# Performance work log

Hardware: AMD Instinct MI355X
Metric: run time of the kernel (lower is better)

The kernel has to match this reference:

```python
import jax, jax.numpy as jnp
import numpy as np
import math

B, A, T = 64, 23, 128          # batch, num_agents, max seq len
D, AE, S, H = 256, 32, 6, 8    # d_model, agent_encoding_dim, static_dim, heads
DK = D // H                     # 32
DM = D + AE                     # 288, MHA q/k/v dim
NEG = -1e10                     # masked_fill constant from source


def sinusoidal_pe(pos, d):
    # pos: int array [...], returns [..., d] standard transformer PE at positions pos
    half = jnp.arange(d // 2, dtype=jnp.float32)
    div = jnp.exp(-half * (math.log(10000.0) * 2.0 / d))          # [d/2]
    ang = pos[..., None].astype(jnp.float32) * div                # [..., d/2]
    return jnp.stack([jnp.sin(ang), jnp.cos(ang)], axis=-1).reshape(*pos.shape, d)


def setup_inputs() -> dict:
    key = jax.random.key(0)
    ks = jax.random.split(key, 20)
    std = 0.02
    data = jax.random.normal(ks[0], (B, A, T), jnp.float32)
    lengths = jax.random.randint(ks[1], (B, A), 0, T + 1).astype(jnp.int32)   # mask arg = lengths
    t = jnp.arange(T, dtype=jnp.int32)
    time = jnp.where(t[None, None, :] < lengths[:, :, None], t[None, None, :], -1)  # [B,A,T], -1 = pad
    static = jax.random.normal(ks[2], (B, S), jnp.float32)
    # per-agent Linear(1, D): weight [A, D], bias [A, D]
    W_embed = std * jax.random.normal(ks[3], (A, D), jnp.float32)
    b_embed = std * jax.random.normal(ks[4], (A, D), jnp.float32)
    E_var = std * jax.random.normal(ks[5], (A, AE), jnp.float32)            # VariateEncoding table
    W_static = std * jax.random.normal(ks[6], (S, D), jnp.float32)
    b_static = jnp.zeros((D,), jnp.float32)
    Wq = std * jax.random.normal(ks[7], (DM, D), jnp.float32); bq = jnp.zeros((D,), jnp.float32)
    Wk = std * jax.random.normal(ks[8], (DM, D), jnp.float32); bk = jnp.zeros((D,), jnp.float32)
    Wv = std * jax.random.normal(ks[9], (DM, D), jnp.float32); bv = jnp.zeros((D,), jnp.float32)
    Wo = std * jax.random.normal(ks[10], (D, DM), jnp.float32); bo = jnp.zeros((DM,), jnp.float32)
    Wg = std * jax.random.normal(ks[11], (DM + D, 1), jnp.float32); bg = jnp.zeros((1,), jnp.float32)
    return dict(data=data, time=time, mask=lengths, static=static,
                W_embed=W_embed, b_embed=b_embed, E_var=E_var,
                W_static=W_static, b_static=b_static,
                Wq=Wq, bq=bq, Wk=Wk, bk=bk, Wv=Wv, bv=bv, Wo=Wo, bo=bo,
                Wg=Wg, bg=bg)


def reference(data, time, mask, static, W_embed, b_embed, E_var, W_static, b_static,
              Wq, bq, Wk, bk, Wv, bv, Wo, bo, Wg, bg):
    lengths = mask                                            # [B,A] sequence lengths
    t = jnp.arange(T)
    valid = t[None, None, :] < lengths[:, :, None]            # [B,A,T] bool
    # mask_matrix[i,:len,:len]=1 double loop -> vectorized outer product
    mask4 = valid[:, :, :, None] & valid[:, :, None, :]       # [B,A,T,T]

    # per-agent Linear(1, D) loop -> batched rank-1 affine, then ReLU
    data_embeds = jax.nn.relu(data[..., None] * W_embed[None, :, None, :]
                              + b_embed[None, :, None, :])    # [B,A,T,D]

    # src_pe: sinusoidal positional encoding at (clamped) time values
    pe = sinusoidal_pe(jnp.maximum(time, 0), D)               # [B,A,T,D]
    src = data_embeds + pe

    # variate (agent-id) embedding concat -> [B,A,T,D+AE]; encoder = identity
    var = jnp.broadcast_to(E_var[None, :, None, :], (B, A, T, AE))
    memory = jnp.concatenate([src, var], axis=-1)             # [B,A,T,DM]

    # time-masked mean pool over T
    time_mask = time >= 0                                     # [B,A,T]
    memory = jnp.where(time_mask[..., None], memory, 0.0)
    counts = time_mask.sum(axis=2).astype(memory.dtype)       # [B,A]
    agentwise = memory.sum(axis=2) / (counts[..., None] + 1e-9)  # [B,A,DM]

    # custom MHA (dim='Time'): q_len = 1 per agent, keys/values over T
    q = jnp.einsum('bae,ed->bad', agentwise, Wq) + bq          # [B,A,D]
    k = jnp.einsum('bate,ed->batd', memory, Wk) + bk           # [B,A,T,D]
    v = jnp.einsum('bate,ed->batd', memory, Wv) + bv
    qh = q.reshape(B, A, H, DK)                                # [B,A,H,DK] (q_len=1 squeezed)
    kh = k.reshape(B, A, T, H, DK).transpose(0, 1, 3, 2, 4)    # [B,A,H,T,DK]
    vh = v.reshape(B, A, T, H, DK).transpose(0, 1, 3, 2, 4)
    scores = jnp.einsum('bahd,bahtd->baht', qh, kh) / math.sqrt(DK)  # [B,A,H,T]
    amask = mask4[:, :, 0, :]                                  # [B,A,T] row 0 of per-agent mask
    scores = jnp.where(amask[:, :, None, :], scores, NEG)
    p = jax.nn.softmax(scores, axis=-1)                        # dropout = eval (identity)
    ctx = jnp.einsum('baht,bahtd->bahd', p, vh).reshape(B, A, D)
    agent_feat = jnp.einsum('bad,de->bae', ctx, Wo) + bo       # [B,A,DM]

    # agent-masked mean pool over agents
    agent_mask = counts > 0                                    # [B,A]
    agent_feat = jnp.where(agent_mask[..., None], agent_feat, 0.0)
    denom = agent_mask.sum(axis=1).astype(agent_feat.dtype) + 1e-9
    aggre = agent_feat.sum(axis=1) / denom[:, None]            # [B,DM]

    static_feat = static @ W_static + b_static                 # [B,D]
    all_feature = jnp.concatenate([aggre, static_feat], axis=-1)  # [B,DM+D]
    return all_feature @ Wg + bg                               # [B,1]


if __name__ == '__main__':
    out = reference(**setup_inputs())
    print(out.shape, jnp.asarray(out).dtype)
```

## Files before the change

### kernel.cpp

```cpp
#include <hip/hip_runtime.h>
#include <math.h>

#define NB 64
#define NA 23
#define NT 128
#define ND 256
#define NAE 32
#define NS 6
#define NH 8
#define NDM 288

#define OFF_PET    0
#define OFF_PECUM  32768
#define OFF_WKT    65792
#define OFF_VWO    131328
#define OFF_CST    133632
#define OFF_S      133648

__global__ __launch_bounds__(256) void setup_kernel(
    const float* __restrict__ Wk, const float* __restrict__ Wv,
    const float* __restrict__ Wo, const float* __restrict__ Wg,
    const float* __restrict__ bv, const float* __restrict__ bo,
    const float* __restrict__ W_static, const float* __restrict__ b_static,
    const float* __restrict__ bg, float* __restrict__ ws)
{
    const int blk = blockIdx.x;
    const int tid = threadIdx.x;
    float* peT   = ws + OFF_PET;
    float* PEcum = ws + OFF_PECUM;
    float* WkT   = ws + OFF_WKT;
    float* VWo   = ws + OFF_VWO;
    float* cst   = ws + OFF_CST;

    if (blk < 128) {
        const int g = tid >> 7, t = tid & 127;
        const int e = blk * 2 + g;
        const int i = e >> 1;
        const float kdiv = 0.07195578415606394f;
        const float dv = expf(-(float)i * kdiv);
        const float ang = (float)t * dv;
        const float v = (e & 1) ? cosf(ang) : sinf(ang);
        peT[e * NT + t] = v;
        __shared__ float buf[256];
        buf[tid] = v;
        #pragma unroll
        for (int s = 1; s < 128; s <<= 1) {
            __syncthreads();
            float add = (t >= s) ? buf[tid - s] : 0.f;
            __syncthreads();
            buf[tid] += add;
        }
        __syncthreads();
        PEcum[(t + 1) * ND + e] = buf[tid];
    } else if (blk < 384) {
        const int j = blk - 128;
        const float scale = 0.17677669529663687f;
        WkT[j * 256 + tid] = Wk[tid * ND + j] * scale;
    } else if (blk < 392) {
        const int h = blk - 384;
        __shared__ float wog[32];
        {
            const int jj = tid >> 3, sub = tid & 7;
            const int j = h * 32 + jj;
            float acc = 0.f;
            const int m0 = sub * 36;
            #pragma unroll 4
            for (int m = m0; m < m0 + 36; ++m)
                acc = fmaf(Wo[j * NDM + m], Wg[m], acc);
            acc += __shfl_down(acc, 4, 8);
            acc += __shfl_down(acc, 2, 8);
            acc += __shfl_down(acc, 1, 8);
            if (sub == 0) wog[jj] = acc;
        }
        __syncthreads();
        for (int e = tid; e < NDM; e += 256) {
            float acc = 0.f;
            #pragma unroll 8
            for (int jj = 0; jj < 32; ++jj)
                acc = fmaf(Wv[e * ND + h * 32 + jj], wog[jj], acc);
            VWo[h * NDM + e] = acc;
        }
        if (tid == 0) {
            float acc = 0.f;
            #pragma unroll 8
            for (int jj = 0; jj < 32; ++jj)
                acc = fmaf(bv[h * 32 + jj], wog[jj], acc);
            cst[8 + h] = acc;
        }
    } else {
        const int i = tid >> 5, sub = tid & 31;
        float acc = 0.f;
        if (i < 6) {
            for (int m = sub; m < 256; m += 32)
                acc = fmaf(W_static[i * ND + m], Wg[NDM + m], acc);
        } else if (i == 6) {
            for (int m = sub; m < 256; m += 32)
                acc = fmaf(b_static[m], Wg[NDM + m], acc);
        } else {
            for (int m = sub; m < NDM; m += 32)
                acc = fmaf(bo[m], Wg[m], acc);
        }
        #pragma unroll
        for (int off = 16; off > 0; off >>= 1)
            acc += __shfl_down(acc, off, 32);
        if (sub == 0) cst[i] = (i == 6) ? acc + bg[0] : acc;
    }
}

__global__ __launch_bounds__(256) void main_kernel(
    const float* __restrict__ data, const int* __restrict__ lengths,
    const float* __restrict__ W_embed, const float* __restrict__ b_embed,
    const float* __restrict__ E_var,
    const float* __restrict__ Wq, const float* __restrict__ bq,
    float* __restrict__ ws)
{
    const int wg = blockIdx.x;
    const int a = wg % NA;
    const int tid = threadIdx.x;
    const int L = lengths[wg];

    if (L == 0) {
        if (tid == 0) ws[OFF_S + wg] = 0.f;
        return;
    }

    __shared__ float xs[NT];
    __shared__ float agentwise[NDM];
    __shared__ float qs[ND];
    __shared__ float2 Wb[ND];
    __shared__ __align__(16) float combo[ND * 16];
    __shared__ float evvS[NH];
    __shared__ float red[4];

    const float* peT   = ws + OFF_PET;
    const float* PEcum = ws + OFF_PECUM;
    const float* WkT   = ws + OFF_WKT;
    const float* VWo   = ws + OFF_VWO;
    const float* cstp  = ws + OFF_CST;

    if (tid < NT) xs[tid] = data[wg * NT + tid];
    __syncthreads();
    {
        const int e = tid;
        const float We = W_embed[a * ND + e];
        const float be = b_embed[a * ND + e];
        Wb[e] = make_float2(We, be);
        float acc = 0.f;
        #pragma unroll 4
        for (int t = 0; t < L; ++t)
            acc += fmaxf(fmaf(xs[t], We, be), 0.f);
        agentwise[e] = (acc + PEcum[L * ND + e]) / (float)L;
    }
    if (tid < NAE) agentwise[ND + tid] = E_var[a * NAE + tid];
    __syncthreads();

    {
        const int j = tid;
        float acc = bq[j];
        #pragma unroll 4
        for (int f = 0; f < NDM; ++f)
            acc = fmaf(agentwise[f], Wq[f * ND + j], acc);
        qs[j] = acc;
    }
    __syncthreads();

    {
        const int h = tid >> 5, eo = tid & 31;
        const float* wr = WkT + (h * 32) * 256;
        for (int eb = 0; eb < 8; ++eb) {
            const int e = eb * 32 + eo;
            float acc = 0.f;
            #pragma unroll 8
            for (int j = 0; j < 32; ++j)
                acc = fmaf(wr[j * 256 + e], qs[h * 32 + j], acc);
            combo[e * 16 + h] = acc;
        }
    }
    for (int idx = tid; idx < NH * ND; idx += 256) {
        const int h = idx >> 8, e = idx & 255;
        combo[e * 16 + 8 + h] = VWo[h * NDM + e];
    }
    {
        const int h = tid >> 5, ee = tid & 31;
        float v = E_var[a * NAE + ee] * VWo[h * NDM + ND + ee];
        v += __shfl_down(v, 16, 32);
        v += __shfl_down(v, 8, 32);
        v += __shfl_down(v, 4, 32);
        v += __shfl_down(v, 2, 32);
        v += __shfl_down(v, 1, 32);
        if (ee == 0) evvS[h] = v;
    }
    __syncthreads();

    {
        const int t = tid & 127;
        const int half = tid >> 7;
        const float xt = xs[t];
        float accS[8], accM[8];
        #pragma unroll
        for (int h = 0; h < 8; ++h) { accS[h] = 0.f; accM[h] = 0.f; }
        const int ebase = half * 128;
        const float4* comboV = (const float4*)combo + ebase * 4;
        const float* peCol = peT + ebase * NT + t;
        #pragma unroll 2
        for (int ee = 0; ee < 128; ++ee) {
            const float2 wb = Wb[ebase + ee];
            const float m = fmaxf(fmaf(xt, wb.x, wb.y), 0.f) + peCol[ee * NT];
            const float4 c0 = comboV[ee * 4 + 0];
            const float4 c1 = comboV[ee * 4 + 1];
            const float4 c2 = comboV[ee * 4 + 2];
            const float4 c3 = comboV[ee * 4 + 3];
            accS[0] = fmaf(m, c0.x, accS[0]);
            accS[1] = fmaf(m, c0.y, accS[1]);
            accS[2] = fmaf(m, c0.z, accS[2]);
            accS[3] = fmaf(m, c0.w, accS[3]);
            accS[4] = fmaf(m, c1.x, accS[4]);
            accS[5] = fmaf(m, c1.y, accS[5]);
            accS[6] = fmaf(m, c1.z, accS[6]);
            accS[7] = fmaf(m, c1.w, accS[7]);
            accM[0] = fmaf(m, c2.x, accM[0]);
            accM[1] = fmaf(m, c2.y, accM[1]);
            accM[2] = fmaf(m, c2.z, accM[2]);
            accM[3] = fmaf(m, c2.w, accM[3]);
            accM[4] = fmaf(m, c3.x, accM[4]);
            accM[5] = fmaf(m, c3.y, accM[5]);
            accM[6] = fmaf(m, c3.z, accM[6]);
            accM[7] = fmaf(m, c3.w, accM[7]);
        }
        __syncthreads();
        float* sc   = combo;
        float* mvb  = combo + 1024;
        float* scP1 = combo + 2048;
        float* mvP1 = combo + 3072;
        if (half == 1) {
            #pragma unroll
            for (int h = 0; h < 8; ++h) {
                scP1[h * NT + t] = accS[h];
                mvP1[h * NT + t] = accM[h];
            }
        }
        __syncthreads();
        if (half == 0) {
            #pragma unroll
            for (int h = 0; h < 8; ++h) {
                sc[h * NT + t]  = accS[h] + scP1[h * NT + t];
                mvb[h * NT + t] = accM[h] + mvP1[h * NT + t];
            }
        }
    }
    __syncthreads();

    {
        const float* sc  = combo;
        const float* mvb = combo + 1024;
        const int wv = tid >> 6, lane = tid & 63;
        float wsum = 0.f;
        for (int hh = 0; hh < 2; ++hh) {
            const int h = wv * 2 + hh;
            float s1 = (lane < L) ? sc[h * NT + lane] : -3e38f;
            float s2 = (lane + 64 < L) ? sc[h * NT + 64 + lane] : -3e38f;
            float mx = fmaxf(s1, s2);
            #pragma unroll
            for (int off = 32; off > 0; off >>= 1)
                mx = fmaxf(mx, __shfl_down(mx, off, 64));
            mx = __shfl(mx, 0, 64);
            const float vbv = evvS[h] + cstp[8 + h];
            float e1 = (lane < L) ? __expf(s1 - mx) : 0.f;
            float e2 = (lane + 64 < L) ? __expf(s2 - mx) : 0.f;
            float num = e1 * (mvb[h * NT + lane] + vbv);
            num = fmaf(e2, mvb[h * NT + 64 + lane] + vbv, num);
            float den = e1 + e2;
            #pragma unroll
            for (int off = 32; off > 0; off >>= 1) {
                num += __shfl_down(num, off, 64);
                den += __shfl_down(den, off, 64);
            }
            if (lane == 0) wsum += num / den;
        }
        if (lane == 0) red[wv] = wsum;
    }
    __syncthreads();
    if (tid == 0) {
        ws[OFF_S + wg] = cstp[7] + red[0] + red[1] + red[2] + red[3];
    }
}

__global__ __launch_bounds__(64) void final_kernel(
    const float* __restrict__ statics, const int* __restrict__ lengths,
    const float* __restrict__ ws, float* __restrict__ out)
{
    const int b = threadIdx.x;
    const float* s_arr = ws + OFF_S;
    const float* cst = ws + OFF_CST;
    float sum = 0.f;
    int n = 0;
    for (int a = 0; a < NA; ++a) {
        if (lengths[b * NA + a] > 0) { sum += s_arr[b * NA + a]; ++n; }
    }
    float o = sum / ((float)n + 1e-9f);
    #pragma unroll
    for (int i = 0; i < NS; ++i)
        o = fmaf(statics[b * NS + i], cst[i], o);
    o += cst[6];
    out[b] = o;
}

extern "C" void kernel_launch(void* const* d_in, const int* in_sizes, int n_in,
                              void* d_out, int out_size, void* d_ws, size_t ws_size,
                              hipStream_t stream) {
    const float* data     = (const float*)d_in[0];
    const int*   mask     = (const int*)d_in[2];
    const float* statics  = (const float*)d_in[3];
    const float* W_embed  = (const float*)d_in[4];
    const float* b_embed  = (const float*)d_in[5];
    const float* E_var    = (const float*)d_in[6];
    const float* W_static = (const float*)d_in[7];
    const float* b_static = (const float*)d_in[8];
    const float* Wq       = (const float*)d_in[9];
    const float* bq       = (const float*)d_in[10];
    const float* Wk       = (const float*)d_in[11];
    const float* Wv       = (const float*)d_in[13];
    const float* bv       = (const float*)d_in[14];
    const float* Wo       = (const float*)d_in[15];
    const float* bo       = (const float*)d_in[16];
    const float* Wg       = (const float*)d_in[17];
    const float* bg       = (const float*)d_in[18];
    float* out = (float*)d_out;
    float* ws  = (float*)d_ws;

    setup_kernel<<<dim3(393), dim3(256), 0, stream>>>(Wk, Wv, Wo, Wg, bv, bo,
                                                      W_static, b_static, bg, ws);
    main_kernel<<<dim3(NB * NA), dim3(256), 0, stream>>>(data, mask, W_embed, b_embed,
                                                         E_var, Wq, bq, ws);
    final_kernel<<<dim3(1), dim3(64), 0, stream>>>(statics, mask, ws, out);
}
```

Before: 169.2 us.

## Split per-agent work into a batched projection pass and a lighter attention pass

Adds a proj_kernel that handles four (batch, agent) pairs per block. It computes the query projection and the K-folded query there, which amortises Wq and WkT reads across agents. The positional encoding contribution is moved out of the inner attention loop: PE·Wk and PE·VWo are precomputed, and the cumulative PE sum is replaced by a closed-form sine-series formula. The attention kernel becomes lighter but now reads per-pair intermediates from global memory, and the sequence grows to four kernel launches.

```diff
diff --git a/kernel.cpp b/kernel.cpp
--- a/kernel.cpp
+++ b/kernel.cpp
@@ -9,53 +9,51 @@
 #define NS 6
 #define NH 8
 #define NDM 288
-
-#define OFF_PET    0
-#define OFF_PECUM  32768
-#define OFF_WKT    65792
-#define OFF_VWO    131328
-#define OFF_CST    133632
-#define OFF_S      133648
-
-__global__ __launch_bounds__(256) void setup_kernel(
-    const float* __restrict__ Wk, const float* __restrict__ Wv,
-    const float* __restrict__ Wo, const float* __restrict__ Wg,
-    const float* __restrict__ bv, const float* __restrict__ bo,
-    const float* __restrict__ W_static, const float* __restrict__ b_static,
-    const float* __restrict__ bg, float* __restrict__ ws)
+#define NBA (NB*NA)
+
+#define OFF_PK     0
+#define OFF_PET    32768
+#define OFF_WKT    65536
+#define OFF_VWO    131072
+#define OFF_QBIAS  133376
+#define OFF_CST    139264
+#define OFF_EVV    139280
+#define OFF_PEM    139464
+#define OFF_QK     140488
+#define OFF_PES    3155144
+#define OFF_S      4662472
+
+#define KDIV  0.07195578415606394f
+#define KSCALE 0.17677669529663687f
+
+__global__ __launch_bounds__(256) void setup1_kernel(
+    const float* __restrict__ Wk, const float* __restrict__ Wq,
+    const float* __restrict__ bq, const float* __restrict__ E_var,
+    const float* __restrict__ Wv, const float* __restrict__ Wo,
+    const float* __restrict__ Wg, const float* __restrict__ bv,
+    const float* __restrict__ bo, const float* __restrict__ W_static,
+    const float* __restrict__ b_static, const float* __restrict__ bg,
+    float* __restrict__ ws)
 {
-    const int blk = blockIdx.x;
-    const int tid = threadIdx.x;
-    float* peT   = ws + OFF_PET;
-    float* PEcum = ws + OFF_PECUM;
-    float* WkT   = ws + OFF_WKT;
-    float* VWo   = ws + OFF_VWO;
-    float* cst   = ws + OFF_CST;
-
+    const int blk = blockIdx.x, tid = threadIdx.x;
+    __shared__ float sm[256];
     if (blk < 128) {
-        const int g = tid >> 7, t = tid & 127;
-        const int e = blk * 2 + g;
-        const int i = e >> 1;
-        const float kdiv = 0.07195578415606394f;
-        const float dv = expf(-(float)i * kdiv);
+        const int t = blk;
+        const int e = tid, i = e >> 1;
+        const float dv = __expf(-(float)i * KDIV);
         const float ang = (float)t * dv;
         const float v = (e & 1) ? cosf(ang) : sinf(ang);
-        peT[e * NT + t] = v;
-        __shared__ float buf[256];
-        buf[tid] = v;
-        #pragma unroll
-        for (int s = 1; s < 128; s <<= 1) {
-            __syncthreads();
-            float add = (t >= s) ? buf[tid - s] : 0.f;
-            __syncthreads();
-            buf[tid] += add;
-        }
-        __syncthreads();
-        PEcum[(t + 1) * ND + e] = buf[tid];
+        sm[e] = v;
+        ws[OFF_PET + e * NT + t] = v;
+        __syncthreads();
+        float acc = 0.f;
+        #pragma unroll 4
+        for (int e2 = 0; e2 < 256; ++e2)
+            acc = fmaf(sm[e2], Wk[e2 * ND + tid], acc);
+        ws[OFF_PK + tid * NT + t] = acc * KSCALE;
     } else if (blk < 384) {
         const int j = blk - 128;
-        const float scale = 0.17677669529663687f;
-        WkT[j * 256 + tid] = Wk[tid * ND + j] * scale;
+        ws[OFF_WKT + j * 256 + tid] = Wk[tid * ND + j] * KSCALE;
     } else if (blk < 392) {
         const int h = blk - 384;
         __shared__ float wog[32];
@@ -78,154 +76,222 @@
             #pragma unroll 8
             for (int jj = 0; jj < 32; ++jj)
                 acc = fmaf(Wv[e * ND + h * 32 + jj], wog[jj], acc);
-            VWo[h * NDM + e] = acc;
-        }
-        if (tid == 0) {
+            ws[OFF_VWO + h * NDM + e] = acc;
+        }
+    } else if (blk < 415) {
+        const int a = blk - 392;
+        float acc = bq[tid];
+        #pragma unroll 8
+        for (int ee = 0; ee < NAE; ++ee)
+            acc = fmaf(E_var[a * NAE + ee], Wq[(256 + ee) * ND + tid], acc);
+        ws[OFF_QBIAS + a * ND + tid] = acc;
+    } else {
+        float acc = 0.f;
+        const float* row = Wo + tid * NDM;
+        for (int m = 0; m < NDM; ++m) acc = fmaf(row[m], Wg[m], acc);
+        sm[tid] = acc;
+        __syncthreads();
+        const int i = tid >> 5, sub = tid & 31;
+        float v = 0.f;
+        if (i < 6) { for (int m = sub; m < 256; m += 32) v = fmaf(W_static[i * ND + m], Wg[NDM + m], v); }
+        else if (i == 6) { for (int m = sub; m < 256; m += 32) v = fmaf(b_static[m], Wg[NDM + m], v); }
+        else { for (int m = sub; m < NDM; m += 32) v = fmaf(bo[m], Wg[m], v); }
+        #pragma unroll
+        for (int off = 16; off > 0; off >>= 1) v += __shfl_down(v, off, 32);
+        if (sub == 0) ws[OFF_CST + i] = (i == 6) ? v + bg[0] : v;
+        {
+            const int h = i, jj = sub;
+            float u = bv[h * 32 + jj] * sm[h * 32 + jj];
+            #pragma unroll
+            for (int off = 16; off > 0; off >>= 1) u += __shfl_down(u, off, 32);
+            if (sub == 0) ws[OFF_CST + 8 + h] = u;
+        }
+    }
+}
+
+__global__ __launch_bounds__(256) void proj_kernel(
+    const float* __restrict__ data, const int* __restrict__ lengths,
+    const float* __restrict__ W_embed, const float* __restrict__ b_embed,
+    const float* __restrict__ E_var, const float* __restrict__ Wq,
+    float* ws)
+{
+    const int blk = blockIdx.x, tid = threadIdx.x;
+    if (blk < 368) {
+        __shared__ __align__(16) float sm[4608];
+        float*  X    = sm;
+        float2* Wb4  = (float2*)(sm + 512);
+        float*  agwS = sm + 512 + 2048;
+        float*  qS   = agwS + 1024;
+        const int wg4 = blk * 4;
+        int aa[4], La[4];
+        #pragma unroll
+        for (int i = 0; i < 4; ++i) { aa[i] = (wg4 + i) % NA; La[i] = lengths[wg4 + i]; }
+        if (tid < 128) {
+            #pragma unroll
+            for (int i = 0; i < 4; ++i) X[i * 128 + tid] = data[(wg4 + i) * NT + tid];
+        }
+        #pragma unroll
+        for (int i = 0; i < 4; ++i)
+            Wb4[i * 256 + tid] = make_float2(W_embed[aa[i] * ND + tid], b_embed[aa[i] * ND + tid]);
+        __syncthreads();
+        {
+            const int e = tid;
+            const int ii = e >> 1;
+            const float dv = __expf(-(float)ii * KDIV);
+            const float hd = 0.5f * dv;
+            float agw[4];
+            #pragma unroll
+            for (int i = 0; i < 4; ++i) {
+                const float2 wb = Wb4[i * 256 + e];
+                const int Li = La[i];
+                float acc = 0.f;
+                #pragma unroll 4
+                for (int t = 0; t < Li; ++t)
+                    acc += fmaxf(fmaf(X[i * 128 + t], wb.x, wb.y), 0.f);
+                float r = 0.f;
+                if (Li > 0) {
+                    const float s1 = sinf((float)Li * hd);
+                    const float a2 = (float)(Li - 1) * hd;
+                    const float num = (e & 1) ? cosf(a2) : sinf(a2);
+                    const float pec = num * s1 / sinf(hd);
+                    r = (acc + pec) / (float)Li;
+                }
+                agw[i] = r;
+            }
+            *(float4*)&agwS[e * 4] = make_float4(agw[0], agw[1], agw[2], agw[3]);
+        }
+        __syncthreads();
+        {
+            const int j = tid;
+            float4 acc = make_float4(ws[OFF_QBIAS + aa[0] * ND + j], ws[OFF_QBIAS + aa[1] * ND + j],
+                                     ws[OFF_QBIAS + aa[2] * ND + j], ws[OFF_QBIAS + aa[3] * ND + j]);
+            #pragma unroll 4
+            for (int f = 0; f < 256; ++f) {
+                const float w = Wq[f * ND + j];
+                const float4 ag = *(const float4*)&agwS[f * 4];
+                acc.x = fmaf(ag.x, w, acc.x); acc.y = fmaf(ag.y, w, acc.y);
+                acc.z = fmaf(ag.z, w, acc.z); acc.w = fmaf(ag.w, w, acc.w);
+            }
+            *(float4*)&qS[j * 4] = acc;
+        }
+        __syncthreads();
+        {
+            const int e = tid;
+            for (int h = 0; h < 8; ++h) {
+                float4 acc = make_float4(0.f, 0.f, 0.f, 0.f);
+                #pragma unroll 8
+                for (int j = 0; j < 32; ++j) {
+                    const int jj = h * 32 + j;
+                    const float w = ws[OFF_WKT + jj * 256 + e];
+                    const float4 qv = *(const float4*)&qS[jj * 4];
+                    acc.x = fmaf(qv.x, w, acc.x); acc.y = fmaf(qv.y, w, acc.y);
+                    acc.z = fmaf(qv.z, w, acc.z); acc.w = fmaf(qv.w, w, acc.w);
+                }
+                ws[OFF_QK + (size_t)(wg4 + 0) * 2048 + h * 256 + e] = acc.x;
+                ws[OFF_QK + (size_t)(wg4 + 1) * 2048 + h * 256 + e] = acc.y;
+                ws[OFF_QK + (size_t)(wg4 + 2) * 2048 + h * 256 + e] = acc.z;
+                ws[OFF_QK + (size_t)(wg4 + 3) * 2048 + h * 256 + e] = acc.w;
+            }
+        }
+        {
+            const int t = tid & 127, hg = tid >> 7;
+            float accS[4][4];
+            #pragma unroll
+            for (int p = 0; p < 4; ++p)
+                #pragma unroll
+                for (int i = 0; i < 4; ++i) accS[p][i] = 0.f;
+            #pragma unroll
+            for (int p = 0; p < 4; ++p) {
+                const int h = hg * 4 + p;
+                #pragma unroll 4
+                for (int j = 0; j < 32; ++j) {
+                    const int jj = h * 32 + j;
+                    const float pk = ws[OFF_PK + jj * NT + t];
+                    const float4 qv = *(const float4*)&qS[jj * 4];
+                    accS[p][0] = fmaf(qv.x, pk, accS[p][0]);
+                    accS[p][1] = fmaf(qv.y, pk, accS[p][1]);
+                    accS[p][2] = fmaf(qv.z, pk, accS[p][2]);
+                    accS[p][3] = fmaf(qv.w, pk, accS[p][3]);
+                }
+            }
+            #pragma unroll
+            for (int p = 0; p < 4; ++p) {
+                const int h = hg * 4 + p;
+                #pragma unroll
+                for (int i = 0; i < 4; ++i)
+                    ws[OFF_PES + (size_t)(wg4 + i) * 1024 + h * 128 + t] = accS[p][i];
+            }
+        }
+    } else if (blk < 372) {
+        const int h = (blk - 368) * 2 + (tid >> 7);
+        const int t = tid & 127;
+        float acc = 0.f;
+        #pragma unroll 4
+        for (int e = 0; e < 256; ++e)
+            acc = fmaf(ws[OFF_PET + e * NT + t], ws[OFF_VWO + h * NDM + e], acc);
+        ws[OFF_PEM + h * NT + t] = acc;
+    } else {
+        if (tid < 184) {
+            const int a = tid >> 3, h = tid & 7;
             float acc = 0.f;
             #pragma unroll 8
-            for (int jj = 0; jj < 32; ++jj)
-                acc = fmaf(bv[h * 32 + jj], wog[jj], acc);
-            cst[8 + h] = acc;
-        }
-    } else {
-        const int i = tid >> 5, sub = tid & 31;
-        float acc = 0.f;
-        if (i < 6) {
-            for (int m = sub; m < 256; m += 32)
-                acc = fmaf(W_static[i * ND + m], Wg[NDM + m], acc);
-        } else if (i == 6) {
-            for (int m = sub; m < 256; m += 32)
-                acc = fmaf(b_static[m], Wg[NDM + m], acc);
-        } else {
-            for (int m = sub; m < NDM; m += 32)
-                acc = fmaf(bo[m], Wg[m], acc);
-        }
-        #pragma unroll
-        for (int off = 16; off > 0; off >>= 1)
-            acc += __shfl_down(acc, off, 32);
-        if (sub == 0) cst[i] = (i == 6) ? acc + bg[0] : acc;
+            for (int ee = 0; ee < NAE; ++ee)
+                acc = fmaf(E_var[a * NAE + ee], ws[OFF_VWO + h * NDM + 256 + ee], acc);
+            ws[OFF_EVV + tid] = acc;
+        }
     }
 }
 
-__global__ __launch_bounds__(256) void main_kernel(
+__global__ __launch_bounds__(256) void ef_kernel(
     const float* __restrict__ data, const int* __restrict__ lengths,
     const float* __restrict__ W_embed, const float* __restrict__ b_embed,
-    const float* __restrict__ E_var,
-    const float* __restrict__ Wq, const float* __restrict__ bq,
-    float* __restrict__ ws)
+    float* ws)
 {
-    const int wg = blockIdx.x;
+    const int wg = blockIdx.x, tid = threadIdx.x;
     const int a = wg % NA;
-    const int tid = threadIdx.x;
     const int L = lengths[wg];
-
-    if (L == 0) {
-        if (tid == 0) ws[OFF_S + wg] = 0.f;
-        return;
-    }
-
-    __shared__ float xs[NT];
-    __shared__ float agentwise[NDM];
-    __shared__ float qs[ND];
-    __shared__ float2 Wb[ND];
-    __shared__ __align__(16) float combo[ND * 16];
-    __shared__ float evvS[NH];
+    if (L == 0) { if (tid == 0) ws[OFF_S + wg] = 0.f; return; }
+
+    __shared__ __align__(16) float combo[4096];
+    __shared__ float xs[128];
+    __shared__ float2 Wb[256];
     __shared__ float red[4];
 
-    const float* peT   = ws + OFF_PET;
-    const float* PEcum = ws + OFF_PECUM;
-    const float* WkT   = ws + OFF_WKT;
-    const float* VWo   = ws + OFF_VWO;
-    const float* cstp  = ws + OFF_CST;
-
-    if (tid < NT) xs[tid] = data[wg * NT + tid];
+    if (tid < 128) xs[tid] = data[wg * NT + tid];
+    Wb[tid] = make_float2(W_embed[a * ND + tid], b_embed[a * ND + tid]);
+    {
+        const float* qkp = ws + OFF_QK + (size_t)wg * 2048;
+        #pragma unroll
+        for (int k = 0; k < 8; ++k) combo[tid * 16 + k] = qkp[k * 256 + tid];
+        #pragma unroll
+        for (int k = 0; k < 8; ++k) combo[tid * 16 + 8 + k] = ws[OFF_VWO + k * NDM + tid];
+    }
     __syncthreads();
+
     {
-        const int e = tid;
-        const float We = W_embed[a * ND + e];
-        const float be = b_embed[a * ND + e];
-        Wb[e] = make_float2(We, be);
-        float acc = 0.f;
-        #pragma unroll 4
-        for (int t = 0; t < L; ++t)
-            acc += fmaxf(fmaf(xs[t], We, be), 0.f);
-        agentwise[e] = (acc + PEcum[L * ND + e]) / (float)L;
-    }
-    if (tid < NAE) agentwise[ND + tid] = E_var[a * NAE + tid];
-    __syncthreads();
-
-    {
-        const int j = tid;
-        float acc = bq[j];
-        #pragma unroll 4
-        for (int f = 0; f < NDM; ++f)
-            acc = fmaf(agentwise[f], Wq[f * ND + j], acc);
-        qs[j] = acc;
-    }
-    __syncthreads();
-
-    {
-        const int h = tid >> 5, eo = tid & 31;
-        const float* wr = WkT + (h * 32) * 256;
-        for (int eb = 0; eb < 8; ++eb) {
-            const int e = eb * 32 + eo;
-            float acc = 0.f;
-            #pragma unroll 8
-            for (int j = 0; j < 32; ++j)
-                acc = fmaf(wr[j * 256 + e], qs[h * 32 + j], acc);
-            combo[e * 16 + h] = acc;
-        }
-    }
-    for (int idx = tid; idx < NH * ND; idx += 256) {
-        const int h = idx >> 8, e = idx & 255;
-        combo[e * 16 + 8 + h] = VWo[h * NDM + e];
-    }
-    {
-        const int h = tid >> 5, ee = tid & 31;
-        float v = E_var[a * NAE + ee] * VWo[h * NDM + ND + ee];
-        v += __shfl_down(v, 16, 32);
-        v += __shfl_down(v, 8, 32);
-        v += __shfl_down(v, 4, 32);
-        v += __shfl_down(v, 2, 32);
-        v += __shfl_down(v, 1, 32);
-        if (ee == 0) evvS[h] = v;
-    }
-    __syncthreads();
-
-    {
-        const int t = tid & 127;
-        const int half = tid >> 7;
+        const int t = tid & 127, half = tid >> 7;
         const float xt = xs[t];
         float accS[8], accM[8];
         #pragma unroll
         for (int h = 0; h < 8; ++h) { accS[h] = 0.f; accM[h] = 0.f; }
         const int ebase = half * 128;
         const float4* comboV = (const float4*)combo + ebase * 4;
-        const float* peCol = peT + ebase * NT + t;
         #pragma unroll 2
         for (int ee = 0; ee < 128; ++ee) {
             const float2 wb = Wb[ebase + ee];
-            const float m = fmaxf(fmaf(xt, wb.x, wb.y), 0.f) + peCol[ee * NT];
+            const float m = fmaxf(fmaf(xt, wb.x, wb.y), 0.f);
             const float4 c0 = comboV[ee * 4 + 0];
             const float4 c1 = comboV[ee * 4 + 1];
             const float4 c2 = comboV[ee * 4 + 2];
             const float4 c3 = comboV[ee * 4 + 3];
-            accS[0] = fmaf(m, c0.x, accS[0]);
-            accS[1] = fmaf(m, c0.y, accS[1]);
-            accS[2] = fmaf(m, c0.z, accS[2]);
-            accS[3] = fmaf(m, c0.w, accS[3]);
-            accS[4] = fmaf(m, c1.x, accS[4]);
-            accS[5] = fmaf(m, c1.y, accS[5]);
-            accS[6] = fmaf(m, c1.z, accS[6]);
-            accS[7] = fmaf(m, c1.w, accS[7]);
-            accM[0] = fmaf(m, c2.x, accM[0]);
-            accM[1] = fmaf(m, c2.y, accM[1]);
-            accM[2] = fmaf(m, c2.z, accM[2]);
-            accM[3] = fmaf(m, c2.w, accM[3]);
-            accM[4] = fmaf(m, c3.x, accM[4]);
-            accM[5] = fmaf(m, c3.y, accM[5]);
-            accM[6] = fmaf(m, c3.z, accM[6]);
-            accM[7] = fmaf(m, c3.w, accM[7]);
+            accS[0] = fmaf(m, c0.x, accS[0]); accS[1] = fmaf(m, c0.y, accS[1]);
+            accS[2] = fmaf(m, c0.z, accS[2]); accS[3] = fmaf(m, c0.w, accS[3]);
+            accS[4] = fmaf(m, c1.x, accS[4]); accS[5] = fmaf(m, c1.y, accS[5]);
+            accS[6] = fmaf(m, c1.z, accS[6]); accS[7] = fmaf(m, c1.w, accS[7]);
+            accM[0] = fmaf(m, c2.x, accM[0]); accM[1] = fmaf(m, c2.y, accM[1]);
+            accM[2] = fmaf(m, c2.z, accM[2]); accM[3] = fmaf(m, c2.w, accM[3]);
+            accM[4] = fmaf(m, c3.x, accM[4]); accM[5] = fmaf(m, c3.y, accM[5]);
+            accM[6] = fmaf(m, c3.z, accM[6]); accM[7] = fmaf(m, c3.w, accM[7]);
         }
         __syncthreads();
         float* sc   = combo;
@@ -234,17 +300,16 @@
         float* mvP1 = combo + 3072;
         if (half == 1) {
             #pragma unroll
+            for (int h = 0; h < 8; ++h) { scP1[h * 128 + t] = accS[h]; mvP1[h * 128 + t] = accM[h]; }
+        }
+        __syncthreads();
+        if (half == 0) {
+            const float* pes = ws + OFF_PES + (size_t)wg * 1024;
+            const float* pem = ws + OFF_PEM;
+            #pragma unroll
             for (int h = 0; h < 8; ++h) {
-                scP1[h * NT + t] = accS[h];
-                mvP1[h * NT + t] = accM[h];
-            }
-        }
-        __syncthreads();
-        if (half == 0) {
-            #pragma unroll
-            for (int h = 0; h < 8; ++h) {
-                sc[h * NT + t]  = accS[h] + scP1[h * NT + t];
-                mvb[h * NT + t] = accM[h] + mvP1[h * NT + t];
+                sc[h * 128 + t]  = accS[h] + scP1[h * 128 + t] + pes[h * 128 + t];
+                mvb[h * 128 + t] = accM[h] + mvP1[h * 128 + t] + pem[h * 128 + t];
             }
         }
     }
@@ -257,18 +322,18 @@
         float wsum = 0.f;
         for (int hh = 0; hh < 2; ++hh) {
             const int h = wv * 2 + hh;
-            float s1 = (lane < L) ? sc[h * NT + lane] : -3e38f;
-            float s2 = (lane + 64 < L) ? sc[h * NT + 64 + lane] : -3e38f;
+            float s1 = (lane < L) ? sc[h * 128 + lane] : -3e38f;
+            float s2 = (lane + 64 < L) ? sc[h * 128 + 64 + lane] : -3e38f;
             float mx = fmaxf(s1, s2);
             #pragma unroll
             for (int off = 32; off > 0; off >>= 1)
                 mx = fmaxf(mx, __shfl_down(mx, off, 64));
             mx = __shfl(mx, 0, 64);
-            const float vbv = evvS[h] + cstp[8 + h];
+            const float vbv = ws[OFF_EVV + a * 8 + h] + ws[OFF_CST + 8 + h];
             float e1 = (lane < L) ? __expf(s1 - mx) : 0.f;
             float e2 = (lane + 64 < L) ? __expf(s2 - mx) : 0.f;
-            float num = e1 * (mvb[h * NT + lane] + vbv);
-            num = fmaf(e2, mvb[h * NT + 64 + lane] + vbv, num);
+            float num = e1 * (mvb[h * 128 + lane] + vbv);
+            num = fmaf(e2, mvb[h * 128 + 64 + lane] + vbv, num);
             float den = e1 + e2;
             #pragma unroll
             for (int off = 32; off > 0; off >>= 1) {
@@ -280,9 +345,8 @@
         if (lane == 0) red[wv] = wsum;
     }
     __syncthreads();
-    if (tid == 0) {
-        ws[OFF_S + wg] = cstp[7] + red[0] + red[1] + red[2] + red[3];
-    }
+    if (tid == 0)
+        ws[OFF_S + wg] = ws[OFF_CST + 7] + red[0] + red[1] + red[2] + red[3];
 }
 
 __global__ __launch_bounds__(64) void final_kernel(
@@ -328,9 +392,10 @@
     float* out = (float*)d_out;
     float* ws  = (float*)d_ws;
 
-    setup_kernel<<<dim3(393), dim3(256), 0, stream>>>(Wk, Wv, Wo, Wg, bv, bo,
-                                                      W_static, b_static, bg, ws);
-    main_kernel<<<dim3(NB * NA), dim3(256), 0, stream>>>(data, mask, W_embed, b_embed,
-                                                         E_var, Wq, bq, ws);
+    setup1_kernel<<<dim3(416), dim3(256), 0, stream>>>(Wk, Wq, bq, E_var, Wv, Wo, Wg,
+                                                       bv, bo, W_static, b_static, bg, ws);
+    proj_kernel<<<dim3(373), dim3(256), 0, stream>>>(data, mask, W_embed, b_embed,
+                                                     E_var, Wq, ws);
+    ef_kernel<<<dim3(NBA), dim3(256), 0, stream>>>(data, mask, W_embed, b_embed, ws);
     final_kernel<<<dim3(1), dim3(64), 0, stream>>>(statics, mask, ws, out);
 }
```

Measured after the change: 193.9 us. 14.6% more time.
